# Kernel tuning notes

Measured on AMD Instinct MI355X. Metric: run time of the kernel, lower is better.

The kernel has to match this reference:

```python
import jax, jax.numpy as jnp
import numpy as np

N_NODES = 100000
N_EDGES = 3200000
N_GRAPHS = 2048
IN_FEATS = 64
HIDDEN = 128
EXTRA = 8


def setup_inputs() -> dict:
    key = jax.random.key(0)
    ks = jax.random.split(key, 16)
    inp = {
        "feats_node": jax.random.normal(ks[0], (N_NODES, IN_FEATS), jnp.float32),
        "feats_graph": jax.random.normal(ks[1], (N_GRAPHS, EXTRA), jnp.float32),
        "src": jax.random.randint(ks[2], (N_EDGES,), 0, N_NODES, jnp.int32),
        "dst": jax.random.randint(ks[3], (N_EDGES,), 0, N_NODES, jnp.int32),
        "graph_ids": jnp.sort(jax.random.randint(ks[4], (N_NODES,), 0, N_GRAPHS, jnp.int32)),
        # GCN weights (std=0.5 init, zero bias as in the torch module)
        "W1": jax.random.normal(ks[5], (IN_FEATS, HIDDEN), jnp.float32) * 0.5,
        "b1": jnp.zeros((HIDDEN,), jnp.float32),
        "W2": jax.random.normal(ks[6], (HIDDEN, HIDDEN), jnp.float32) * 0.5,
        "b2": jnp.zeros((HIDDEN,), jnp.float32),
        "W3": jax.random.normal(ks[7], (HIDDEN, HIDDEN), jnp.float32) * 0.5,
        "b3": jnp.zeros((HIDDEN,), jnp.float32),
        # MLP: (HIDDEN+EXTRA) -> 2*HIDDEN -> HIDDEN -> 1
        "M1": jax.random.normal(ks[8], (HIDDEN + EXTRA, 2 * HIDDEN), jnp.float32) * 0.5,
        "c1": jnp.zeros((2 * HIDDEN,), jnp.float32),
        "M2": jax.random.normal(ks[9], (2 * HIDDEN, HIDDEN), jnp.float32) * 0.5,
        "c2": jnp.zeros((HIDDEN,), jnp.float32),
        "M3": jax.random.normal(ks[10], (HIDDEN, 1), jnp.float32) * 0.5,
        "c3": jnp.zeros((1,), jnp.float32),
    }
    return inp


def _gcn_layer(h, W, b, src, dst, norm_src, norm_dst):
    # DGL GraphConv, norm='both': h' = D_in^{-1/2} A (D_out^{-1/2} h W) + b
    h = (h * norm_src[:, None]) @ W            # [N, out]
    agg = jax.ops.segment_sum(h[src], dst, num_segments=N_NODES)  # scatter-add over edges
    return agg * norm_dst[:, None] + b


def reference(feats_node, feats_graph, src, dst, graph_ids,
              W1, b1, W2, b2, W3, b3, M1, c1, M2, c2, M3, c3):
    ones_e = jnp.ones((N_EDGES,), jnp.float32)
    out_deg = jax.ops.segment_sum(ones_e, src, num_segments=N_NODES)
    in_deg = jax.ops.segment_sum(ones_e, dst, num_segments=N_NODES)
    norm_src = jax.lax.rsqrt(jnp.maximum(out_deg, 1.0))
    norm_dst = jax.lax.rsqrt(jnp.maximum(in_deg, 1.0))

    h = _gcn_layer(feats_node, W1, b1, src, dst, norm_src, norm_dst)
    h = jax.nn.selu(h)
    h = _gcn_layer(h, W2, b2, src, dst, norm_src, norm_dst)
    h = jax.nn.selu(h)
    h = _gcn_layer(h, W3, b3, src, dst, norm_src, norm_dst)
    h = jax.nn.selu(h)

    # AvgPooling readout: mean node features per graph
    sums = jax.ops.segment_sum(h, graph_ids, num_segments=N_GRAPHS)  # [G, H]
    cnts = jax.ops.segment_sum(jnp.ones((N_NODES,), jnp.float32), graph_ids, num_segments=N_GRAPHS)
    emb = sums / jnp.maximum(cnts, 1.0)[:, None]

    z = jnp.concatenate([emb, feats_graph], axis=1)  # [G, H+EXTRA]
    z = jax.nn.selu(z @ M1 + c1)
    z = jax.nn.selu(z @ M2 + c2)
    return z @ M3 + c3  # [G, 1]
```

## Files before the change

### kernel.cpp

```cpp
#include <hip/hip_runtime.h>
#include <hip/hip_bf16.h>
#include <cstddef>

#define N_NODES 100000
#define N_EDGES 3200000
#define N_GRAPHS 2048
#define IN_FEATS 64
#define HIDDEN 128
#define EXTRA 8

#define SCAN_CHUNK 1024
#define NB_CHUNKS ((N_NODES + SCAN_CHUNK - 1) / SCAN_CHUNK)

#define R_BINS 16000
#define NPASS 7
#define G_SORT 256
#define CHUNK (N_EDGES / G_SORT)

typedef unsigned short bf16_t;
typedef short bfx8 __attribute__((ext_vector_type(8)));
typedef float f32x4 __attribute__((ext_vector_type(4)));

__device__ __forceinline__ float selu_f(float x) {
    const float scale = 1.0507009873554805f;
    const float alpha = 1.6732632423543772f;
    return x > 0.f ? scale * x : scale * alpha * (__expf(x) - 1.f);
}
__device__ __forceinline__ float bf2f(unsigned short u) {
    union { unsigned int i; float f; } c; c.i = ((unsigned int)u) << 16; return c.f;
}
__device__ __forceinline__ unsigned short f2bf(float f) {
    union { float f; unsigned int i; } c; c.f = f;
    unsigned int lsb = (c.i >> 16) & 1;
    c.i += 0x7fffu + lsb;
    return (unsigned short)(c.i >> 16);
}


__global__ __launch_bounds__(512) void histo_kernel(const int* __restrict__ src,
                                                    const int* __restrict__ dst,
                                                    unsigned char* __restrict__ h_src,
                                                    unsigned char* __restrict__ h_dst) {
    __shared__ unsigned int hist[R_BINS];
    const int b = blockIdx.x, t = threadIdx.x;
    const int e0 = b * CHUNK;
#pragma unroll
    for (int ph = 0; ph < 2; ++ph) {
        const int4* key4 = (const int4*)((ph ? src : dst) + e0);
        unsigned char* hout = (ph ? h_src : h_dst) + (size_t)b * N_NODES;
        for (int p = 0; p < NPASS; ++p) {
            const int r0 = p * R_BINS;
            const int rend = min(R_BINS, N_NODES - r0);
            for (int i = t; i < R_BINS; i += 512) hist[i] = 0;
            __syncthreads();
            for (int i = t; i < CHUNK / 4; i += 512) {
                int4 k = key4[i];
                unsigned int x;
                x = (unsigned)(k.x - r0); if (x < (unsigned)R_BINS) atomicAdd(&hist[x], 1u);
                x = (unsigned)(k.y - r0); if (x < (unsigned)R_BINS) atomicAdd(&hist[x], 1u);
                x = (unsigned)(k.z - r0); if (x < (unsigned)R_BINS) atomicAdd(&hist[x], 1u);
                x = (unsigned)(k.w - r0); if (x < (unsigned)R_BINS) atomicAdd(&hist[x], 1u);
            }
            __syncthreads();
            for (int i = t; i < rend; i += 512) hout[r0 + i] = (unsigned char)hist[i];
            __syncthreads();
        }
    }
}

__global__ __launch_bounds__(256) void colsum_kernel(const unsigned char* __restrict__ h_src,
                                                     int* __restrict__ outdeg) {
    int bin = blockIdx.x * 256 + threadIdx.x;
    if (bin >= N_NODES) return;
    int s = 0;
#pragma unroll 8
    for (int b = 0; b < G_SORT; ++b) s += h_src[(size_t)b * N_NODES + bin];
    outdeg[bin] = s;
}

__global__ __launch_bounds__(256) void scanp_kernel(unsigned char* __restrict__ h_dst,
                                                    int* __restrict__ indeg) {
    int bin = blockIdx.x * 256 + threadIdx.x;
    if (bin >= N_NODES) return;
    int run = 0;
#pragma unroll 8
    for (int b = 0; b < G_SORT; ++b) {
        size_t off = (size_t)b * N_NODES + bin;
        int v = h_dst[off];
        h_dst[off] = (unsigned char)run;
        run += v;
    }
    indeg[bin] = run;
}

__global__ __launch_bounds__(512) void sortT_kernel(const int* __restrict__ src,
                                                    const int* __restrict__ dst,
                                                    const unsigned char* __restrict__ h_dst,
                                                    const int* __restrict__ rowptr,
                                                    int* __restrict__ csr_src) {
    __shared__ unsigned int cnt[R_BINS];
    const int b = blockIdx.x, t = threadIdx.x;
    const int e0 = b * CHUNK;
    const int4* d4p = (const int4*)(dst + e0);
    const int4* s4p = (const int4*)(src + e0);
    const unsigned char* hrow = h_dst + (size_t)b * N_NODES;
    for (int p = 0; p < NPASS; ++p) {
        const int r0 = p * R_BINS;
        const unsigned int rend = (unsigned)min(R_BINS, N_NODES - r0);
        for (int i = t; i < (int)rend; i += 512)
            cnt[i] = (unsigned)rowptr[r0 + i] + (unsigned)hrow[r0 + i];
        __syncthreads();
        for (int i = t; i < CHUNK / 4; i += 512) {
            int4 d = d4p[i];
            int4 s = s4p[i];
            unsigned int x;
            x = (unsigned)(d.x - r0); if (x < rend) { unsigned slot = atomicAdd(&cnt[x], 1u); csr_src[slot] = s.x; }
            x = (unsigned)(d.y - r0); if (x < rend) { unsigned slot = atomicAdd(&cnt[x], 1u); csr_src[slot] = s.y; }
            x = (unsigned)(d.z - r0); if (x < rend) { unsigned slot = atomicAdd(&cnt[x], 1u); csr_src[slot] = s.z; }
            x = (unsigned)(d.w - r0); if (x < rend) { unsigned slot = atomicAdd(&cnt[x], 1u); csr_src[slot] = s.w; }
        }
        __syncthreads();
    }
}


__global__ __launch_bounds__(256) void norm_kernel(const int* __restrict__ outdeg,
                                                   const int* __restrict__ indeg,
                                                   float* __restrict__ nsrc,
                                                   float* __restrict__ ndst) {
    int i = blockIdx.x * 256 + threadIdx.x;
    if (i < N_NODES) {
        nsrc[i] = rsqrtf(fmaxf((float)outdeg[i], 1.f));
        ndst[i] = rsqrtf(fmaxf((float)indeg[i], 1.f));
    }
}

__global__ __launch_bounds__(256) void scanA(const int* __restrict__ indeg,
                                             int* __restrict__ partials) {
    __shared__ int red[4];
    const int b = blockIdx.x, t = threadIdx.x;
    int base = b * SCAN_CHUNK + t * 4;
    int s = 0;
#pragma unroll
    for (int k = 0; k < 4; ++k) { int i = base + k; if (i < N_NODES) s += indeg[i]; }
    for (int off = 32; off; off >>= 1) s += __shfl_down(s, off);
    if ((t & 63) == 0) red[t >> 6] = s;
    __syncthreads();
    if (t == 0) partials[b] = red[0] + red[1] + red[2] + red[3];
}

__global__ __launch_bounds__(128) void scanB(int* __restrict__ partials,
                                             int* __restrict__ rowptr) {
    __shared__ int s[128];
    const int t = threadIdx.x;
    int v = (t < NB_CHUNKS) ? partials[t] : 0;
    s[t] = v;
    __syncthreads();
    for (int off = 1; off < 128; off <<= 1) {
        int u = (t >= off) ? s[t - off] : 0;
        __syncthreads();
        s[t] += u;
        __syncthreads();
    }
    if (t < NB_CHUNKS) partials[t] = s[t] - v;
    if (t == 127) rowptr[N_NODES] = s[127];
}

__global__ __launch_bounds__(256) void scanC(const int* __restrict__ indeg,
                                             const int* __restrict__ partials,
                                             int* __restrict__ rowptr) {
    __shared__ int ts[256];
    const int b = blockIdx.x, t = threadIdx.x;
    int base = b * SCAN_CHUNK + t * 4;
    int v[4];
    int s = 0;
#pragma unroll
    for (int k = 0; k < 4; ++k) { int i = base + k; v[k] = (i < N_NODES) ? indeg[i] : 0; s += v[k]; }
    ts[t] = s;
    __syncthreads();
    for (int off = 1; off < 256; off <<= 1) {
        int u = (t >= off) ? ts[t - off] : 0;
        __syncthreads();
        ts[t] += u;
        __syncthreads();
    }
    int excl = ts[t] - s + partials[b];
#pragma unroll
    for (int k = 0; k < 4; ++k) {
        int i = base + k;
        if (i < N_NODES) rowptr[i] = excl;
        excl += v[k];
    }
}

__global__ __launch_bounds__(256) void wprep_kernel(const float* __restrict__ W,
                                                    bf16_t* __restrict__ Wt, int K) {
    int i = blockIdx.x * 256 + threadIdx.x;
    if (i >= 128 * K) return;
    int n = i / K, k = i - n * K;
    Wt[i] = f2bf(W[k * 128 + n]);
}

__global__ __launch_bounds__(256) void prescale_kernel(const float* __restrict__ x,
                                                       const float* __restrict__ nsrc,
                                                       bf16_t* __restrict__ xb) {
    int i = blockIdx.x * 256 + threadIdx.x;
    const int total = N_NODES * (IN_FEATS / 4);
    if (i >= total) return;
    int node = i >> 4;
    float nm = nsrc[node];
    float4 v = ((const float4*)x)[i];
    ushort4 o;
    o.x = f2bf(v.x * nm); o.y = f2bf(v.y * nm);
    o.z = f2bf(v.z * nm); o.w = f2bf(v.w * nm);
    ((ushort4*)xb)[i] = o;
}


__global__ __launch_bounds__(256) void gather64_kernel(const bf16_t* __restrict__ xb,
                                                       const int* __restrict__ rowptr,
                                                       const int* __restrict__ csr_src,
                                                       const float* __restrict__ ndst,
                                                       bf16_t* __restrict__ outb) {
    const int l = threadIdx.x & 63;
    const int q = l >> 4;
    const int s16 = l & 15;
    const int node = (blockIdx.x * 256 + threadIdx.x) >> 6;
    if (node >= N_NODES) return;
    const int r0 = rowptr[node], r1 = rowptr[node + 1];
    float a0 = 0.f, a1 = 0.f, a2 = 0.f, a3 = 0.f;
    for (int base = r0; base < r1; base += 16) {
        const int nb = min(16, r1 - base);
        int myidx = csr_src[base + min(s16, nb - 1)];
#pragma unroll
        for (int j = 0; j < 16; j += 4) {
            if (j >= nb) break;
            int e = j + q;
            int s = __shfl(myidx, min(e, nb - 1));
            if (e < nb) {
                ushort4 u = *(const ushort4*)(xb + (size_t)s * IN_FEATS + s16 * 4);
                a0 += bf2f(u.x); a1 += bf2f(u.y); a2 += bf2f(u.z); a3 += bf2f(u.w);
            }
        }
    }
    a0 += __shfl_xor(a0, 16); a1 += __shfl_xor(a1, 16);
    a2 += __shfl_xor(a2, 16); a3 += __shfl_xor(a3, 16);
    a0 += __shfl_xor(a0, 32); a1 += __shfl_xor(a1, 32);
    a2 += __shfl_xor(a2, 32); a3 += __shfl_xor(a3, 32);
    if (q == 0) {
        float nm = ndst[node];
        ushort4 o;
        o.x = f2bf(a0 * nm); o.y = f2bf(a1 * nm);
        o.z = f2bf(a2 * nm); o.w = f2bf(a3 * nm);
        *(ushort4*)(outb + (size_t)node * IN_FEATS + s16 * 4) = o;
    }
}

__global__ __launch_bounds__(256) void gather128_kernel(const bf16_t* __restrict__ hb,
                                                        const int* __restrict__ rowptr,
                                                        const int* __restrict__ csr_src,
                                                        const float* __restrict__ ndst,
                                                        bf16_t* __restrict__ outb) {
    const int l = threadIdx.x & 63;
    const int half = l >> 5;
    const int sub = l & 31;
    const int node = (blockIdx.x * 256 + threadIdx.x) >> 6;
    if (node >= N_NODES) return;
    const int r0 = rowptr[node], r1 = rowptr[node + 1];
    float a0 = 0.f, a1 = 0.f, a2 = 0.f, a3 = 0.f;
    for (int base = r0; base < r1; base += 32) {
        const int nb = min(32, r1 - base);
        int myidx = csr_src[base + min(sub, nb - 1)];
#pragma unroll 8
        for (int j = 0; j < nb; j += 2) {
            int e = j + half;
            int s = __shfl(myidx, min(e, nb - 1));
            if (e < nb) {
                ushort4 u = *(const ushort4*)(hb + (size_t)s * HIDDEN + sub * 4);
                a0 += bf2f(u.x); a1 += bf2f(u.y); a2 += bf2f(u.z); a3 += bf2f(u.w);
            }
        }
    }
    a0 += __shfl_xor(a0, 32); a1 += __shfl_xor(a1, 32);
    a2 += __shfl_xor(a2, 32); a3 += __shfl_xor(a3, 32);
    if (half == 0) {
        float nm = ndst[node];
        ushort4 o;
        o.x = f2bf(a0 * nm); o.y = f2bf(a1 * nm);
        o.z = f2bf(a2 * nm); o.w = f2bf(a3 * nm);
        *(ushort4*)(outb + (size_t)node * HIDDEN + sub * 4) = o;
    }
}

template <int K, bool SCALE_OUT>
__global__ __launch_bounds__(256) void node_matmul_mfma(const bf16_t* __restrict__ Hb,
                                                        const bf16_t* __restrict__ Wt,
                                                        const float* __restrict__ bias,
                                                        const float* __restrict__ nsrc,
                                                        bf16_t* __restrict__ outb) {
    __shared__ char sW[128 * K * 2];
    const int t = threadIdx.x;

    for (int fb = t * 16; fb < 128 * K * 2; fb += 256 * 16) {
        bfx8 v = *(const bfx8*)((const char*)Wt + fb);
        int n = fb / (2 * K);
        *(bfx8*)(sW + (fb ^ ((n & 7) << 4))) = v;
    }
    __syncthreads();

    const int wv = t >> 6;
    const int l  = t & 63;
    const int m  = l & 15;
    const int kb = l >> 4;
    const int row0 = blockIdx.x * 64 + wv * 16;

    int arow = row0 + m;
    if (arow > N_NODES - 1) arow = N_NODES - 1;
    const char* aptr = (const char*)(Hb + (size_t)arow * K);

    f32x4 acc[8];
#pragma unroll
    for (int f = 0; f < 8; ++f) acc[f] = (f32x4){0.f, 0.f, 0.f, 0.f};

#pragma unroll
    for (int kc = 0; kc < K / 32; ++kc) {
        bfx8 a = *(const bfx8*)(aptr + kc * 64 + kb * 16);
#pragma unroll
        for (int f = 0; f < 8; ++f) {
            int n = f * 16 + m;
            int off = n * (2 * K) + kc * 64 + kb * 16;
            off ^= (n & 7) << 4;
            bfx8 b = *(const bfx8*)(sW + off);
            acc[f] = __builtin_amdgcn_mfma_f32_16x16x32_bf16(a, b, acc[f], 0, 0, 0);
        }
    }

    int nodes[4];
    float nm[4];
#pragma unroll
    for (int j = 0; j < 4; ++j) {
        nodes[j] = row0 + kb * 4 + j;
        nm[j] = 1.f;
        if (SCALE_OUT && nodes[j] < N_NODES) nm[j] = nsrc[nodes[j]];
    }
#pragma unroll
    for (int f = 0; f < 8; ++f) {
        int feat = f * 16 + m;
        float bb = bias[feat];
#pragma unroll
        for (int j = 0; j < 4; ++j) {
            if (nodes[j] < N_NODES) {
                float v = selu_f(acc[f][j] + bb) * nm[j];
                outb[(size_t)nodes[j] * HIDDEN + feat] = f2bf(v);
            }
        }
    }
}

__global__ __launch_bounds__(256) void pool_kernel(const bf16_t* __restrict__ h,
                                                   const int* __restrict__ gid,
                                                   float* __restrict__ emb,
                                                   float* __restrict__ cnt) {
    const int lane = threadIdx.x & 63;
    const int wid = (blockIdx.x * 256 + threadIdx.x) >> 6;
    const int n0 = wid * 64;
    if (n0 >= N_NODES) return;
    const int nend = (n0 + 64 < N_NODES) ? n0 + 64 : N_NODES;
    int cur = gid[n0];
    float ax = 0.f, ay = 0.f, run = 0.f;
    for (int n = n0; n < nend; ++n) {
        int g = gid[n];
        if (g != cur) {
            atomicAdd(&emb[(size_t)cur * HIDDEN + lane * 2], ax);
            atomicAdd(&emb[(size_t)cur * HIDDEN + lane * 2 + 1], ay);
            if (lane == 0) atomicAdd(&cnt[cur], run);
            cur = g; ax = 0.f; ay = 0.f; run = 0.f;
        }
        ushort2 u = *(const ushort2*)(h + (size_t)n * HIDDEN + lane * 2);
        ax += bf2f(u.x); ay += bf2f(u.y);
        run += 1.f;
    }
    atomicAdd(&emb[(size_t)cur * HIDDEN + lane * 2], ax);
    atomicAdd(&emb[(size_t)cur * HIDDEN + lane * 2 + 1], ay);
    if (lane == 0) atomicAdd(&cnt[cur], run);
}

__global__ __launch_bounds__(256) void mlp_kernel(const float* __restrict__ emb,
                                                  const float* __restrict__ cnt,
                                                  const float* __restrict__ fg,
                                                  const float* __restrict__ M1, const float* __restrict__ c1,
                                                  const float* __restrict__ M2, const float* __restrict__ c2,
                                                  const float* __restrict__ M3, const float* __restrict__ c3,
                                                  float* __restrict__ out) {
    const int g = blockIdx.x;
    const int t = threadIdx.x;
    __shared__ float z[HIDDEN + EXTRA];
    __shared__ float z1[2 * HIDDEN];
    __shared__ float z2[HIDDEN];
    if (t < HIDDEN) {
        float c = fmaxf(cnt[g], 1.f);
        z[t] = emb[(size_t)g * HIDDEN + t] / c;
    } else if (t < HIDDEN + EXTRA) {
        z[t] = fg[g * EXTRA + (t - HIDDEN)];
    }
    __syncthreads();
    {
        float s = c1[t];
        for (int k = 0; k < HIDDEN + EXTRA; ++k) s += z[k] * M1[k * (2 * HIDDEN) + t];
        z1[t] = selu_f(s);
    }
    __syncthreads();
    if (t < HIDDEN) {
        float s = c2[t];
        for (int k = 0; k < 2 * HIDDEN; ++k) s += z1[k] * M2[k * HIDDEN + t];
        z2[t] = selu_f(s);
    }
    __syncthreads();
    if (t < 64) {
        float s = z2[t] * M3[t] + z2[t + 64] * M3[t + 64];
#pragma unroll
        for (int off = 32; off; off >>= 1) s += __shfl_down(s, off);
        if (t == 0) out[g] = s + c3[0];
    }
}

extern "C" void kernel_launch(void* const* d_in, const int* in_sizes, int n_in,
                              void* d_out, int out_size, void* d_ws, size_t ws_size,
                              hipStream_t stream) {
    const float* feats_node  = (const float*)d_in[0];
    const float* feats_graph = (const float*)d_in[1];
    const int*   src         = (const int*)d_in[2];
    const int*   dst         = (const int*)d_in[3];
    const int*   gid         = (const int*)d_in[4];
    const float* W1 = (const float*)d_in[5];
    const float* b1 = (const float*)d_in[6];
    const float* W2 = (const float*)d_in[7];
    const float* b2 = (const float*)d_in[8];
    const float* W3 = (const float*)d_in[9];
    const float* b3 = (const float*)d_in[10];
    const float* M1 = (const float*)d_in[11];
    const float* c1 = (const float*)d_in[12];
    const float* M2 = (const float*)d_in[13];
    const float* c2 = (const float*)d_in[14];
    const float* M3 = (const float*)d_in[15];
    const float* c3 = (const float*)d_in[16];
    float* out = (float*)d_out;

    char* ws = (char*)d_ws;
    int* indeg   = (int*)ws;  ws += (size_t)N_NODES * sizeof(int);
    int* outdeg  = (int*)ws;  ws += (size_t)N_NODES * sizeof(int);
    int* rowptr  = (int*)ws;  ws += (size_t)(N_NODES + 4) * sizeof(int);
    int* partials= (int*)ws;  ws += 128 * sizeof(int);
    float* norm_src = (float*)ws; ws += (size_t)N_NODES * sizeof(float);
    float* norm_dst = (float*)ws; ws += (size_t)N_NODES * sizeof(float);
    bf16_t* Wt1 = (bf16_t*)ws; ws += (size_t)128 * IN_FEATS * sizeof(bf16_t);
    bf16_t* Wt2 = (bf16_t*)ws; ws += (size_t)128 * HIDDEN * sizeof(bf16_t);
    bf16_t* Wt3 = (bf16_t*)ws; ws += (size_t)128 * HIDDEN * sizeof(bf16_t);
    int* csr_src = (int*)ws;  ws += (size_t)N_EDGES * sizeof(int);
    bf16_t* bufB = (bf16_t*)ws; ws += (size_t)N_NODES * HIDDEN * sizeof(bf16_t);
    unsigned char* h_dst = (unsigned char*)ws;
    bf16_t* bufA = (bf16_t*)ws;
    ws += (size_t)G_SORT * N_NODES;
    unsigned char* h_src = (unsigned char*)ws;
    bf16_t* xb   = (bf16_t*)ws;
    float* emb   = (float*)(ws + (size_t)N_NODES * IN_FEATS * sizeof(bf16_t));
    float* cnt   = emb + (size_t)N_GRAPHS * HIDDEN;
    ws += (size_t)G_SORT * N_NODES;

    histo_kernel<<<G_SORT, 512, 0, stream>>>(src, dst, h_src, h_dst);
    colsum_kernel<<<(N_NODES + 255) / 256, 256, 0, stream>>>(h_src, outdeg);
    scanp_kernel<<<(N_NODES + 255) / 256, 256, 0, stream>>>(h_dst, indeg);
    scanA<<<NB_CHUNKS, 256, 0, stream>>>(indeg, partials);
    scanB<<<1, 128, 0, stream>>>(partials, rowptr);
    scanC<<<NB_CHUNKS, 256, 0, stream>>>(indeg, partials, rowptr);
    norm_kernel<<<(N_NODES + 255) / 256, 256, 0, stream>>>(outdeg, indeg, norm_src, norm_dst);
    sortT_kernel<<<G_SORT, 512, 0, stream>>>(src, dst, h_dst, rowptr, csr_src);

    wprep_kernel<<<(128 * IN_FEATS + 255) / 256, 256, 0, stream>>>(W1, Wt1, IN_FEATS);
    wprep_kernel<<<(128 * HIDDEN + 255) / 256, 256, 0, stream>>>(W2, Wt2, HIDDEN);
    wprep_kernel<<<(128 * HIDDEN + 255) / 256, 256, 0, stream>>>(W3, Wt3, HIDDEN);
    prescale_kernel<<<(N_NODES * (IN_FEATS / 4) + 255) / 256, 256, 0, stream>>>(feats_node, norm_src, xb);

    const int mm_grid = (N_NODES + 63) / 64;
    const int g_grid  = (N_NODES + 3) / 4;

    gather64_kernel<<<g_grid, 256, 0, stream>>>(xb, rowptr, csr_src, norm_dst, bufA);
    node_matmul_mfma<IN_FEATS, true><<<mm_grid, 256, 0, stream>>>(bufA, Wt1, b1, norm_src, bufB);

    gather128_kernel<<<g_grid, 256, 0, stream>>>(bufB, rowptr, csr_src, norm_dst, bufA);
    node_matmul_mfma<HIDDEN, true><<<mm_grid, 256, 0, stream>>>(bufA, Wt2, b2, norm_src, bufB);

    gather128_kernel<<<g_grid, 256, 0, stream>>>(bufB, rowptr, csr_src, norm_dst, bufA);
    node_matmul_mfma<HIDDEN, false><<<mm_grid, 256, 0, stream>>>(bufA, Wt3, b3, norm_src, bufB);

    hipMemsetAsync(emb, 0, ((size_t)N_GRAPHS * HIDDEN + N_GRAPHS) * sizeof(float), stream);
    const int n_waves = (N_NODES + 63) / 64;
    pool_kernel<<<(n_waves + 3) / 4, 256, 0, stream>>>(bufB, gid, emb, cnt);
    mlp_kernel<<<N_GRAPHS, 256, 0, stream>>>(emb, cnt, feats_graph,
                                             M1, c1, M2, c2, M3, c3, out);
}
```

Measured before the change: 693.3 us.

## Reorder GCN to matmul-then-gather with feature-paneled layout

```diff
diff --git a/kernel.cpp b/kernel.cpp
--- a/kernel.cpp
+++ b/kernel.cpp
@@ -216,88 +216,55 @@
     ((ushort4*)xb)[i] = o;
 }
 
-
-__global__ __launch_bounds__(256) void gather64_kernel(const bf16_t* __restrict__ xb,
-                                                       const int* __restrict__ rowptr,
-                                                       const int* __restrict__ csr_src,
-                                                       const float* __restrict__ ndst,
-                                                       bf16_t* __restrict__ outb) {
+template <bool SCALE_OUT>
+__global__ __launch_bounds__(256) void gatherP_kernel(const bf16_t* __restrict__ hP,
+                                                      const int* __restrict__ rowptr,
+                                                      const int* __restrict__ csr_src,
+                                                      const float* __restrict__ ndst,
+                                                      const float* __restrict__ nsrc,
+                                                      const float* __restrict__ bias,
+                                                      bf16_t* __restrict__ outP) {
+    const int p = blockIdx.x & 7;
+    const int node = (((blockIdx.x >> 3) * 256) + threadIdx.x) >> 6;
+    if (node >= N_NODES) return;
     const int l = threadIdx.x & 63;
-    const int q = l >> 4;
-    const int s16 = l & 15;
-    const int node = (blockIdx.x * 256 + threadIdx.x) >> 6;
-    if (node >= N_NODES) return;
+    const int g = l >> 3;
+    const int k = l & 7;
+    const bf16_t* bp = hP + (size_t)p * N_NODES * 16;
     const int r0 = rowptr[node], r1 = rowptr[node + 1];
-    float a0 = 0.f, a1 = 0.f, a2 = 0.f, a3 = 0.f;
-    for (int base = r0; base < r1; base += 16) {
-        const int nb = min(16, r1 - base);
-        int myidx = csr_src[base + min(s16, nb - 1)];
-#pragma unroll
-        for (int j = 0; j < 16; j += 4) {
+    float a0 = 0.f, a1 = 0.f;
+    for (int base = r0; base < r1; base += 64) {
+        const int nb = min(64, r1 - base);
+        int myidx = csr_src[base + min(l, nb - 1)];
+#pragma unroll
+        for (int j = 0; j < 64; j += 8) {
             if (j >= nb) break;
-            int e = j + q;
+            int e = j + g;
             int s = __shfl(myidx, min(e, nb - 1));
             if (e < nb) {
-                ushort4 u = *(const ushort4*)(xb + (size_t)s * IN_FEATS + s16 * 4);
-                a0 += bf2f(u.x); a1 += bf2f(u.y); a2 += bf2f(u.z); a3 += bf2f(u.w);
+                ushort2 u = *(const ushort2*)(bp + (size_t)s * 16 + k * 2);
+                a0 += bf2f(u.x); a1 += bf2f(u.y);
             }
         }
     }
+    a0 += __shfl_xor(a0, 8);  a1 += __shfl_xor(a1, 8);
     a0 += __shfl_xor(a0, 16); a1 += __shfl_xor(a1, 16);
-    a2 += __shfl_xor(a2, 16); a3 += __shfl_xor(a3, 16);
     a0 += __shfl_xor(a0, 32); a1 += __shfl_xor(a1, 32);
-    a2 += __shfl_xor(a2, 32); a3 += __shfl_xor(a3, 32);
-    if (q == 0) {
-        float nm = ndst[node];
-        ushort4 o;
-        o.x = f2bf(a0 * nm); o.y = f2bf(a1 * nm);
-        o.z = f2bf(a2 * nm); o.w = f2bf(a3 * nm);
-        *(ushort4*)(outb + (size_t)node * IN_FEATS + s16 * 4) = o;
-    }
-}
-
-__global__ __launch_bounds__(256) void gather128_kernel(const bf16_t* __restrict__ hb,
-                                                        const int* __restrict__ rowptr,
-                                                        const int* __restrict__ csr_src,
-                                                        const float* __restrict__ ndst,
-                                                        bf16_t* __restrict__ outb) {
-    const int l = threadIdx.x & 63;
-    const int half = l >> 5;
-    const int sub = l & 31;
-    const int node = (blockIdx.x * 256 + threadIdx.x) >> 6;
-    if (node >= N_NODES) return;
-    const int r0 = rowptr[node], r1 = rowptr[node + 1];
-    float a0 = 0.f, a1 = 0.f, a2 = 0.f, a3 = 0.f;
-    for (int base = r0; base < r1; base += 32) {
-        const int nb = min(32, r1 - base);
-        int myidx = csr_src[base + min(sub, nb - 1)];
-#pragma unroll 8
-        for (int j = 0; j < nb; j += 2) {
-            int e = j + half;
-            int s = __shfl(myidx, min(e, nb - 1));
-            if (e < nb) {
-                ushort4 u = *(const ushort4*)(hb + (size_t)s * HIDDEN + sub * 4);
-                a0 += bf2f(u.x); a1 += bf2f(u.y); a2 += bf2f(u.z); a3 += bf2f(u.w);
-            }
-        }
-    }
-    a0 += __shfl_xor(a0, 32); a1 += __shfl_xor(a1, 32);
-    a2 += __shfl_xor(a2, 32); a3 += __shfl_xor(a3, 32);
-    if (half == 0) {
-        float nm = ndst[node];
-        ushort4 o;
-        o.x = f2bf(a0 * nm); o.y = f2bf(a1 * nm);
-        o.z = f2bf(a2 * nm); o.w = f2bf(a3 * nm);
-        *(ushort4*)(outb + (size_t)node * HIDDEN + sub * 4) = o;
-    }
-}
-
-template <int K, bool SCALE_OUT>
+    if (g == 0) {
+        const float nm = ndst[node];
+        const int f0 = p * 16 + k * 2;
+        float v0 = selu_f(a0 * nm + bias[f0]);
+        float v1 = selu_f(a1 * nm + bias[f0 + 1]);
+        if (SCALE_OUT) { float sc = nsrc[node]; v0 *= sc; v1 *= sc; }
+        ushort2 o; o.x = f2bf(v0); o.y = f2bf(v1);
+        *(ushort2*)(outP + ((size_t)p * N_NODES + node) * 16 + k * 2) = o;
+    }
+}
+
+template <int K, bool A_PANEL>
 __global__ __launch_bounds__(256) void node_matmul_mfma(const bf16_t* __restrict__ Hb,
                                                         const bf16_t* __restrict__ Wt,
-                                                        const float* __restrict__ bias,
-                                                        const float* __restrict__ nsrc,
-                                                        bf16_t* __restrict__ outb) {
+                                                        bf16_t* __restrict__ outP) {
     __shared__ char sW[128 * K * 2];
     const int t = threadIdx.x;
 
@@ -316,7 +283,6 @@
 
     int arow = row0 + m;
     if (arow > N_NODES - 1) arow = N_NODES - 1;
-    const char* aptr = (const char*)(Hb + (size_t)arow * K);
 
     f32x4 acc[8];
 #pragma unroll
@@ -324,7 +290,15 @@
 
 #pragma unroll
     for (int kc = 0; kc < K / 32; ++kc) {
-        bfx8 a = *(const bfx8*)(aptr + kc * 64 + kb * 16);
+        const char* ap;
+        if (A_PANEL) {
+            int fb = kc * 64 + kb * 16;
+            int pp = fb >> 5;
+            ap = (const char*)Hb + ((size_t)pp * N_NODES + arow) * 32 + (fb & 31);
+        } else {
+            ap = (const char*)(Hb + (size_t)arow * K) + kc * 64 + kb * 16;
+        }
+        bfx8 a = *(const bfx8*)ap;
 #pragma unroll
         for (int f = 0; f < 8; ++f) {
             int n = f * 16 + m;
@@ -335,29 +309,18 @@
         }
     }
 
-    int nodes[4];
-    float nm[4];
-#pragma unroll
-    for (int j = 0; j < 4; ++j) {
-        nodes[j] = row0 + kb * 4 + j;
-        nm[j] = 1.f;
-        if (SCALE_OUT && nodes[j] < N_NODES) nm[j] = nsrc[nodes[j]];
-    }
 #pragma unroll
     for (int f = 0; f < 8; ++f) {
-        int feat = f * 16 + m;
-        float bb = bias[feat];
+        bf16_t* op = outP + (size_t)f * N_NODES * 16 + m;
 #pragma unroll
         for (int j = 0; j < 4; ++j) {
-            if (nodes[j] < N_NODES) {
-                float v = selu_f(acc[f][j] + bb) * nm[j];
-                outb[(size_t)nodes[j] * HIDDEN + feat] = f2bf(v);
-            }
-        }
-    }
-}
-
-__global__ __launch_bounds__(256) void pool_kernel(const bf16_t* __restrict__ h,
+            int node = row0 + kb * 4 + j;
+            if (node < N_NODES) op[(size_t)node * 16] = f2bf(acc[f][j]);
+        }
+    }
+}
+
+__global__ __launch_bounds__(256) void pool_kernel(const bf16_t* __restrict__ hP,
                                                    const int* __restrict__ gid,
                                                    float* __restrict__ emb,
                                                    float* __restrict__ cnt) {
@@ -366,6 +329,7 @@
     const int n0 = wid * 64;
     if (n0 >= N_NODES) return;
     const int nend = (n0 + 64 < N_NODES) ? n0 + 64 : N_NODES;
+    const bf16_t* bp = hP + (size_t)(lane >> 3) * N_NODES * 16 + (lane & 7) * 2;
     int cur = gid[n0];
     float ax = 0.f, ay = 0.f, run = 0.f;
     for (int n = n0; n < nend; ++n) {
@@ -376,7 +340,7 @@
             if (lane == 0) atomicAdd(&cnt[cur], run);
             cur = g; ax = 0.f; ay = 0.f; run = 0.f;
         }
-        ushort2 u = *(const ushort2*)(h + (size_t)n * HIDDEN + lane * 2);
+        ushort2 u = *(const ushort2*)(bp + (size_t)n * 16);
         ax += bf2f(u.x); ay += bf2f(u.y);
         run += 1.f;
     }
@@ -482,20 +446,20 @@
     prescale_kernel<<<(N_NODES * (IN_FEATS / 4) + 255) / 256, 256, 0, stream>>>(feats_node, norm_src, xb);
 
     const int mm_grid = (N_NODES + 63) / 64;
-    const int g_grid  = (N_NODES + 3) / 4;
-
-    gather64_kernel<<<g_grid, 256, 0, stream>>>(xb, rowptr, csr_src, norm_dst, bufA);
-    node_matmul_mfma<IN_FEATS, true><<<mm_grid, 256, 0, stream>>>(bufA, Wt1, b1, norm_src, bufB);
-
-    gather128_kernel<<<g_grid, 256, 0, stream>>>(bufB, rowptr, csr_src, norm_dst, bufA);
-    node_matmul_mfma<HIDDEN, true><<<mm_grid, 256, 0, stream>>>(bufA, Wt2, b2, norm_src, bufB);
-
-    gather128_kernel<<<g_grid, 256, 0, stream>>>(bufB, rowptr, csr_src, norm_dst, bufA);
-    node_matmul_mfma<HIDDEN, false><<<mm_grid, 256, 0, stream>>>(bufA, Wt3, b3, norm_src, bufB);
+    const int gp_grid = 8 * ((N_NODES + 3) / 4);
+
+    node_matmul_mfma<IN_FEATS, false><<<mm_grid, 256, 0, stream>>>(xb, Wt1, bufB);
+    gatherP_kernel<true><<<gp_grid, 256, 0, stream>>>(bufB, rowptr, csr_src, norm_dst, norm_src, b1, bufA);
+
+    node_matmul_mfma<HIDDEN, true><<<mm_grid, 256, 0, stream>>>(bufA, Wt2, bufB);
+    gatherP_kernel<true><<<gp_grid, 256, 0, stream>>>(bufB, rowptr, csr_src, norm_dst, norm_src, b2, bufA);
+
+    node_matmul_mfma<HIDDEN, true><<<mm_grid, 256, 0, stream>>>(bufA, Wt3, bufB);
+    gatherP_kernel<false><<<gp_grid, 256, 0, stream>>>(bufB, rowptr, csr_src, norm_dst, norm_src, b3, bufA);
 
     hipMemsetAsync(emb, 0, ((size_t)N_GRAPHS * HIDDEN + N_GRAPHS) * sizeof(float), stream);
     const int n_waves = (N_NODES + 63) / 64;
-    pool_kernel<<<(n_waves + 3) / 4, 256, 0, stream>>>(bufB, gid, emb, cnt);
+    pool_kernel<<<(n_waves + 3) / 4, 256, 0, stream>>>(bufA, gid, emb, cnt);
     mlp_kernel<<<N_GRAPHS, 256, 0, stream>>>(emb, cnt, feats_graph,
                                              M1, c1, M2, c2, M3, c3, out);
 }
```

Measured after the change: 1.132 ms. 63.3% more time.

## Pack byte histograms in LDS to cut radix passes and fuse degree kernels

Applied to the files above, without the earlier changes.

```diff
diff --git a/kernel.cpp b/kernel.cpp
--- a/kernel.cpp
+++ b/kernel.cpp
@@ -12,8 +12,8 @@
 #define SCAN_CHUNK 1024
 #define NB_CHUNKS ((N_NODES + SCAN_CHUNK - 1) / SCAN_CHUNK)
 
-#define R_BINS 16000
-#define NPASS 7
+#define R_BINS 64000
+#define NPASS 2
 #define G_SORT 256
 #define CHUNK (N_EDGES / G_SORT)
 
@@ -41,7 +41,7 @@
                                                     const int* __restrict__ dst,
                                                     unsigned char* __restrict__ h_src,
                                                     unsigned char* __restrict__ h_dst) {
-    __shared__ unsigned int hist[R_BINS];
+    __shared__ unsigned int hist[R_BINS / 4];
     const int b = blockIdx.x, t = threadIdx.x;
     const int e0 = b * CHUNK;
 #pragma unroll
@@ -51,37 +51,35 @@
         for (int p = 0; p < NPASS; ++p) {
             const int r0 = p * R_BINS;
             const int rend = min(R_BINS, N_NODES - r0);
-            for (int i = t; i < R_BINS; i += 512) hist[i] = 0;
+            for (int i = t; i < R_BINS / 4; i += 512) hist[i] = 0;
             __syncthreads();
             for (int i = t; i < CHUNK / 4; i += 512) {
                 int4 k = key4[i];
                 unsigned int x;
-                x = (unsigned)(k.x - r0); if (x < (unsigned)R_BINS) atomicAdd(&hist[x], 1u);
-                x = (unsigned)(k.y - r0); if (x < (unsigned)R_BINS) atomicAdd(&hist[x], 1u);
-                x = (unsigned)(k.z - r0); if (x < (unsigned)R_BINS) atomicAdd(&hist[x], 1u);
-                x = (unsigned)(k.w - r0); if (x < (unsigned)R_BINS) atomicAdd(&hist[x], 1u);
+                x = (unsigned)(k.x - r0); if (x < (unsigned)R_BINS) atomicAdd(&hist[x >> 2], 1u << ((x & 3) << 3));
+                x = (unsigned)(k.y - r0); if (x < (unsigned)R_BINS) atomicAdd(&hist[x >> 2], 1u << ((x & 3) << 3));
+                x = (unsigned)(k.z - r0); if (x < (unsigned)R_BINS) atomicAdd(&hist[x >> 2], 1u << ((x & 3) << 3));
+                x = (unsigned)(k.w - r0); if (x < (unsigned)R_BINS) atomicAdd(&hist[x >> 2], 1u << ((x & 3) << 3));
             }
             __syncthreads();
-            for (int i = t; i < rend; i += 512) hout[r0 + i] = (unsigned char)hist[i];
+            unsigned int* ho4 = (unsigned int*)(hout + r0);
+            for (int i = t; i < rend / 4; i += 512) ho4[i] = hist[i];
             __syncthreads();
         }
     }
 }
 
-__global__ __launch_bounds__(256) void colsum_kernel(const unsigned char* __restrict__ h_src,
-                                                     int* __restrict__ outdeg) {
+__global__ __launch_bounds__(256) void degs_kernel(const unsigned char* __restrict__ h_src,
+                                                   unsigned char* __restrict__ h_dst,
+                                                   int* __restrict__ indeg,
+                                                   float* __restrict__ nsrc,
+                                                   float* __restrict__ ndst) {
     int bin = blockIdx.x * 256 + threadIdx.x;
     if (bin >= N_NODES) return;
     int s = 0;
 #pragma unroll 8
     for (int b = 0; b < G_SORT; ++b) s += h_src[(size_t)b * N_NODES + bin];
-    outdeg[bin] = s;
-}
-
-__global__ __launch_bounds__(256) void scanp_kernel(unsigned char* __restrict__ h_dst,
-                                                    int* __restrict__ indeg) {
-    int bin = blockIdx.x * 256 + threadIdx.x;
-    if (bin >= N_NODES) return;
+    nsrc[bin] = rsqrtf(fmaxf((float)s, 1.f));
     int run = 0;
 #pragma unroll 8
     for (int b = 0; b < G_SORT; ++b) {
@@ -91,6 +89,7 @@
         run += v;
     }
     indeg[bin] = run;
+    ndst[bin] = rsqrtf(fmaxf((float)run, 1.f));
 }
 
 __global__ __launch_bounds__(512) void sortT_kernel(const int* __restrict__ src,
@@ -98,7 +97,7 @@
                                                     const unsigned char* __restrict__ h_dst,
                                                     const int* __restrict__ rowptr,
                                                     int* __restrict__ csr_src) {
-    __shared__ unsigned int cnt[R_BINS];
+    __shared__ unsigned int cnt[R_BINS / 4];
     const int b = blockIdx.x, t = threadIdx.x;
     const int e0 = b * CHUNK;
     const int4* d4p = (const int4*)(dst + e0);
@@ -106,34 +105,43 @@
     const unsigned char* hrow = h_dst + (size_t)b * N_NODES;
     for (int p = 0; p < NPASS; ++p) {
         const int r0 = p * R_BINS;
-        const unsigned int rend = (unsigned)min(R_BINS, N_NODES - r0);
-        for (int i = t; i < (int)rend; i += 512)
-            cnt[i] = (unsigned)rowptr[r0 + i] + (unsigned)hrow[r0 + i];
+        const int rend = min(R_BINS, N_NODES - r0);
+        const unsigned int* hr4 = (const unsigned int*)(hrow + r0);
+        for (int i = t; i < rend / 4; i += 512) cnt[i] = hr4[i];
         __syncthreads();
         for (int i = t; i < CHUNK / 4; i += 512) {
             int4 d = d4p[i];
             int4 s = s4p[i];
-            unsigned int x;
-            x = (unsigned)(d.x - r0); if (x < rend) { unsigned slot = atomicAdd(&cnt[x], 1u); csr_src[slot] = s.x; }
-            x = (unsigned)(d.y - r0); if (x < rend) { unsigned slot = atomicAdd(&cnt[x], 1u); csr_src[slot] = s.y; }
-            x = (unsigned)(d.z - r0); if (x < rend) { unsigned slot = atomicAdd(&cnt[x], 1u); csr_src[slot] = s.z; }
-            x = (unsigned)(d.w - r0); if (x < rend) { unsigned slot = atomicAdd(&cnt[x], 1u); csr_src[slot] = s.w; }
+            unsigned int x, old, rank;
+            x = (unsigned)(d.x - r0);
+            if (x < (unsigned)R_BINS) {
+                old = atomicAdd(&cnt[x >> 2], 1u << ((x & 3) << 3));
+                rank = (old >> ((x & 3) << 3)) & 0xffu;
+                csr_src[rowptr[d.x] + rank] = s.x;
+            }
+            x = (unsigned)(d.y - r0);
+            if (x < (unsigned)R_BINS) {
+                old = atomicAdd(&cnt[x >> 2], 1u << ((x & 3) << 3));
+                rank = (old >> ((x & 3) << 3)) & 0xffu;
+                csr_src[rowptr[d.y] + rank] = s.y;
+            }
+            x = (unsigned)(d.z - r0);
+            if (x < (unsigned)R_BINS) {
+                old = atomicAdd(&cnt[x >> 2], 1u << ((x & 3) << 3));
+                rank = (old >> ((x & 3) << 3)) & 0xffu;
+                csr_src[rowptr[d.z] + rank] = s.z;
+            }
+            x = (unsigned)(d.w - r0);
+            if (x < (unsigned)R_BINS) {
+                old = atomicAdd(&cnt[x >> 2], 1u << ((x & 3) << 3));
+                rank = (old >> ((x & 3) << 3)) & 0xffu;
+                csr_src[rowptr[d.w] + rank] = s.w;
+            }
         }
         __syncthreads();
     }
 }
 
-
-__global__ __launch_bounds__(256) void norm_kernel(const int* __restrict__ outdeg,
-                                                   const int* __restrict__ indeg,
-                                                   float* __restrict__ nsrc,
-                                                   float* __restrict__ ndst) {
-    int i = blockIdx.x * 256 + threadIdx.x;
-    if (i < N_NODES) {
-        nsrc[i] = rsqrtf(fmaxf((float)outdeg[i], 1.f));
-        ndst[i] = rsqrtf(fmaxf((float)indeg[i], 1.f));
-    }
-}
 
 __global__ __launch_bounds__(256) void scanA(const int* __restrict__ indeg,
                                              int* __restrict__ partials) {
@@ -215,7 +223,6 @@
     o.z = f2bf(v.z * nm); o.w = f2bf(v.w * nm);
     ((ushort4*)xb)[i] = o;
 }
-
 
 __global__ __launch_bounds__(256) void gather64_kernel(const bf16_t* __restrict__ xb,
                                                        const int* __restrict__ rowptr,
@@ -231,7 +238,7 @@
     float a0 = 0.f, a1 = 0.f, a2 = 0.f, a3 = 0.f;
     for (int base = r0; base < r1; base += 16) {
         const int nb = min(16, r1 - base);
-        int myidx = csr_src[base + min(s16, nb - 1)];
+        int myidx = __builtin_nontemporal_load(&csr_src[base + min(s16, nb - 1)]);
 #pragma unroll
         for (int j = 0; j < 16; j += 4) {
             if (j >= nb) break;
@@ -270,7 +277,7 @@
     float a0 = 0.f, a1 = 0.f, a2 = 0.f, a3 = 0.f;
     for (int base = r0; base < r1; base += 32) {
         const int nb = min(32, r1 - base);
-        int myidx = csr_src[base + min(sub, nb - 1)];
+        int myidx = __builtin_nontemporal_load(&csr_src[base + min(sub, nb - 1)]);
 #pragma unroll 8
         for (int j = 0; j < nb; j += 2) {
             int e = j + half;
@@ -448,7 +455,6 @@
 
     char* ws = (char*)d_ws;
     int* indeg   = (int*)ws;  ws += (size_t)N_NODES * sizeof(int);
-    int* outdeg  = (int*)ws;  ws += (size_t)N_NODES * sizeof(int);
     int* rowptr  = (int*)ws;  ws += (size_t)(N_NODES + 4) * sizeof(int);
     int* partials= (int*)ws;  ws += 128 * sizeof(int);
     float* norm_src = (float*)ws; ws += (size_t)N_NODES * sizeof(float);
@@ -468,12 +474,10 @@
     ws += (size_t)G_SORT * N_NODES;
 
     histo_kernel<<<G_SORT, 512, 0, stream>>>(src, dst, h_src, h_dst);
-    colsum_kernel<<<(N_NODES + 255) / 256, 256, 0, stream>>>(h_src, outdeg);
-    scanp_kernel<<<(N_NODES + 255) / 256, 256, 0, stream>>>(h_dst, indeg);
+    degs_kernel<<<(N_NODES + 255) / 256, 256, 0, stream>>>(h_src, h_dst, indeg, norm_src, norm_dst);
     scanA<<<NB_CHUNKS, 256, 0, stream>>>(indeg, partials);
     scanB<<<1, 128, 0, stream>>>(partials, rowptr);
     scanC<<<NB_CHUNKS, 256, 0, stream>>>(indeg, partials, rowptr);
-    norm_kernel<<<(N_NODES + 255) / 256, 256, 0, stream>>>(outdeg, indeg, norm_src, norm_dst);
     sortT_kernel<<<G_SORT, 512, 0, stream>>>(src, dst, h_dst, rowptr, csr_src);
 
     wprep_kernel<<<(128 * IN_FEATS + 255) / 256, 256, 0, stream>>>(W1, Wt1, IN_FEATS);
```

Result: faster. 646.8 us (-6.7%).
